# Optimization experiments

Measured on AMD Instinct MI355X. Metric: run time of the kernel, lower is better.

The kernel has to match this reference:

```python
import jax, jax.numpy as jnp
import numpy as np

TOP_K = 5
TEMPERATURE = 0.1
EPS = 1e-12


def _normalize(x):
    # F.normalize(x, dim=-1): x / max(||x||, eps)
    n = jnp.linalg.norm(x, axis=-1, keepdims=True)
    return x / jnp.maximum(n, EPS)


def setup_inputs() -> dict:
    key = jax.random.key(0)
    k1, k2, k3 = jax.random.split(key, 3)
    B, N, D = 1024, 200000, 128
    query = jax.random.normal(k1, (B, D), dtype=jnp.float32)
    # memory bank stores L2-normalized keys (MemoryBank.build applies F.normalize)
    memory = _normalize(jax.random.normal(k2, (N, D), dtype=jnp.float32))
    index_map = jnp.arange(N, dtype=jnp.int64)
    exclude_indices = jax.random.randint(k3, (B,), 0, N, dtype=jnp.int64)
    return {"query": query, "memory": memory, "index_map": index_map,
            "exclude_indices": exclude_indices}


def reference(query, memory, index_map, exclude_indices):
    # cosine similarity: normalize query, memory is already normalized
    qn = _normalize(query)                       # [B, D]
    sim = qn @ memory.T                          # [B, N]
    # exclude own training sample (training-time self-exclusion)
    mask = exclude_indices[:, None] == index_map[None, :]   # [B, N]
    sim = jnp.where(mask, -jnp.inf, sim)
    # top-k (effective_top_k = min(top_k, N-1) = TOP_K here)
    top_sim, top_idx = jax.lax.top_k(sim, TOP_K)             # [B, K]
    weights = jax.nn.softmax(top_sim / TEMPERATURE, axis=-1)  # [B, K]
    vecs = memory[top_idx]                                   # [B, K, D]
    retrieved = jnp.einsum('bk,bkd->bd', weights, vecs)      # weighted sum
    retrieved = _normalize(retrieved)
    distances = 1.0 - top_sim[:, 0]                          # [B]
    return retrieved, distances, weights
```

## Files before the change

### kernel.cpp

```cpp
#include <hip/hip_runtime.h>
#include <hip/hip_bf16.h>
#include <math.h>

#define D128 128
#define TOPK 5
#define NP 200704
#define NCH2 12544
#define NSTRIP 392
#define MARGIN 0.008f
#define CAP 1024
#define SCAP 96
#define SCST 34

typedef __attribute__((ext_vector_type(8))) short short8;
typedef __attribute__((ext_vector_type(4))) float f32x4;

__device__ __forceinline__ short f2bf(float f) {
    union { float f; unsigned u; } c; c.f = f;
    unsigned u = c.u + 0x7FFFu + ((c.u >> 16) & 1u);
    return (short)(u >> 16);
}

__device__ __forceinline__ unsigned pkbf(float x, float y) {
    __hip_bfloat162 h = __float22bfloat162_rn(make_float2(x, y));
    unsigned u; __builtin_memcpy(&u, &h, 4);
    return u;
}
__device__ __forceinline__ unsigned pkh(float a, float b) {
    union { _Float16 h[2]; unsigned u; } c;
    c.h[0] = (_Float16)a; c.h[1] = (_Float16)b; return c.u;
}

template <int NN>
__device__ __forceinline__ void insertg(float (&v)[NN], int (&x)[NN], float nv, int nj) {
    bool g[NN];
    #pragma unroll
    for (int i = 0; i < NN; ++i) g[i] = nv > v[i];
    #pragma unroll
    for (int i = NN - 1; i > 0; --i) {
        v[i] = g[i - 1] ? v[i - 1] : (g[i] ? nv : v[i]);
        x[i] = g[i - 1] ? x[i - 1] : (g[i] ? nj : x[i]);
    }
    v[0] = g[0] ? nv : v[0];
    x[0] = g[0] ? nj : x[0];
}
template <int NN>
__device__ __forceinline__ void insertv(float (&v)[NN], float nv) {
    bool g[NN];
    #pragma unroll
    for (int i = 0; i < NN; ++i) g[i] = nv > v[i];
    #pragma unroll
    for (int i = NN - 1; i > 0; --i)
        v[i] = g[i - 1] ? v[i - 1] : (g[i] ? nv : v[i]);
    v[0] = g[0] ? nv : v[0];
}

__global__ void qnorm_kernel(const float* __restrict__ q, float* __restrict__ qn,
                             short* __restrict__ qbf) {
    int b = blockIdx.x, t = threadIdx.x;
    float v0 = q[(size_t)b * D128 + t];
    float v1 = q[(size_t)b * D128 + t + 64];
    float ss = v0 * v0 + v1 * v1;
    #pragma unroll
    for (int off = 32; off > 0; off >>= 1) ss += __shfl_xor(ss, off, 64);
    float scale = 1.0f / fmaxf(sqrtf(ss), 1e-12f);
    float a0 = v0 * scale, a1 = v1 * scale;
    qn[(size_t)b * D128 + t] = a0;
    qn[(size_t)b * D128 + t + 64] = a1;
    qbf[(size_t)b * D128 + t] = f2bf(a0);
    qbf[(size_t)b * D128 + t + 64] = f2bf(a1);
}

#define MFMA16(a, b, c) __builtin_amdgcn_mfma_f32_16x16x32_bf16(a, b, c, 0, 0, 0)

__global__ __launch_bounds__(256, 3) void simtopk_max(
    const short* __restrict__ qbf, const float* __restrict__ mem,
    _Float16* __restrict__ candT, _Float16* __restrict__ stripT, int N) {
    __shared__ short sK[2][64 * 136];
    __shared__ _Float16 sC[256 * SCST];
    const int b = blockIdx.x;
    const int strip = (b & 7) + ((b >> 5) << 3);
    const int qsg = (b >> 3) & 3;
    const int t = threadIdx.x, w = t >> 6, lane = t & 63;
    const int n = lane & 15, quad = lane >> 4;
    const bool qb0 = (quad & 1) != 0, qb1 = (quad & 2) != 0;
    const int qbase = qsg * 256 + w * 64;

    short8 bq[4][4];
    #pragma unroll
    for (int f = 0; f < 4; ++f) {
        const short* qrow = qbf + (size_t)(qbase + f * 16 + n) * D128 + quad * 8;
        #pragma unroll
        for (int s = 0; s < 4; ++s) bq[f][s] = *(const short8*)(qrow + s * 32);
    }

    const size_t k0 = (size_t)strip * 512;
    const int srow = t >> 4, scol = t & 15;
    const float* gbase = mem + (k0 + srow) * (size_t)D128 + scol * 8;
    const bool tail = (k0 + 512 > (size_t)N);

    float4 fa[8];

    auto loadg = [&](int g) {
        const float* base = gbase + (size_t)g * 64 * D128;
        #pragma unroll
        for (int i = 0; i < 4; ++i) {
            const float4* p = (const float4*)(base + (size_t)i * 16 * D128);
            if (tail) {
                size_t key = k0 + (size_t)(g * 64 + srow + i * 16);
                if (key >= (size_t)N) p = (const float4*)mem;
            }
            fa[2 * i]     = p[0];
            fa[2 * i + 1] = p[1];
        }
    };
    auto storesk = [&](int g, int buf) {
        #pragma unroll
        for (int i = 0; i < 4; ++i) {
            uint4 wv;
            wv.x = pkbf(fa[2 * i].x,     fa[2 * i].y);
            wv.y = pkbf(fa[2 * i].z,     fa[2 * i].w);
            wv.z = pkbf(fa[2 * i + 1].x, fa[2 * i + 1].y);
            wv.w = pkbf(fa[2 * i + 1].z, fa[2 * i + 1].w);
            if (tail && (k0 + (size_t)(g * 64 + srow + i * 16) >= (size_t)N))
                wv = make_uint4(0, 0, 0, 0);
            *((uint4*)&sK[buf][(srow + 16 * i) * 136 + scol * 8]) = wv;
        }
    };

    loadg(0);
    storesk(0, 0);
    __syncthreads();
    loadg(1);

    const int qloc = w * 64 + quad * 16 + n;
    unsigned* sCrow = (unsigned*)((char*)sC + qloc * (SCST * 2));

    for (int round = 0; round < 8; ++round) {
        if (round < 7) storesk(round + 1, (round + 1) & 1);
        if (round < 6) loadg(round + 2);

        const short* kb = sK[round & 1];
        float fin[4];
        #pragma unroll
        for (int tt = 0; tt < 4; ++tt) {
            const short* ab = &kb[(tt * 16 + n) * 136 + quad * 8];
            short8 a0 = *(const short8*)(ab);
            short8 a1 = *(const short8*)(ab + 32);
            short8 a2 = *(const short8*)(ab + 64);
            short8 a3 = *(const short8*)(ab + 96);
            f32x4 c0 = {0.f, 0.f, 0.f, 0.f}, c1 = c0, c2 = c0, c3 = c0;
            c0 = MFMA16(a0, bq[0][0], c0);
            c1 = MFMA16(a0, bq[1][0], c1);
            c2 = MFMA16(a0, bq[2][0], c2);
            c3 = MFMA16(a0, bq[3][0], c3);
            c0 = MFMA16(a1, bq[0][1], c0);
            c1 = MFMA16(a1, bq[1][1], c1);
            c2 = MFMA16(a1, bq[2][1], c2);
            c3 = MFMA16(a1, bq[3][1], c3);
            c0 = MFMA16(a2, bq[0][2], c0);
            c1 = MFMA16(a2, bq[1][2], c1);
            c2 = MFMA16(a2, bq[2][2], c2);
            c3 = MFMA16(a2, bq[3][2], c3);
            c0 = MFMA16(a3, bq[0][3], c0);
            c1 = MFMA16(a3, bq[1][3], c1);
            c2 = MFMA16(a3, bq[2][3], c2);
            c3 = MFMA16(a3, bq[3][3], c3);
            float m0 = fmaxf(fmaxf(c0[0], c0[1]), fmaxf(c0[2], c0[3]));
            float m1 = fmaxf(fmaxf(c1[0], c1[1]), fmaxf(c1[2], c1[3]));
            float m2 = fmaxf(fmaxf(c2[0], c2[1]), fmaxf(c2[2], c2[3]));
            float m3 = fmaxf(fmaxf(c3[0], c3[1]), fmaxf(c3[2], c3[3]));
            float u0 = qb0 ? m1 : m0, u1 = qb0 ? m0 : m1;
            float u2 = qb0 ? m3 : m2, u3 = qb0 ? m2 : m3;
            float v0 = qb1 ? u2 : u0, v1 = qb1 ? u3 : u1;
            float v2 = qb1 ? u0 : u2, v3 = qb1 ? u1 : u3;
            float A = fmaxf(v0, __shfl_xor(v2, 32, 64));
            float B = fmaxf(v1, __shfl_xor(v3, 32, 64));
            fin[tt] = fmaxf(A, __shfl_xor(B, 16, 64));
        }
        sCrow[round * 2]     = pkh(fin[0], fin[1]);
        sCrow[round * 2 + 1] = pkh(fin[2], fin[3]);
        __syncthreads();
    }

    {
        int q = qsg * 256 + t;
        unsigned* gdst = (unsigned*)((short*)candT + (size_t)q * NCH2 + strip * 32);
        const unsigned* row = (const unsigned*)((const char*)sC + t * (SCST * 2));
        float mx = -3e38f;
        #pragma unroll
        for (int j = 0; j < 4; ++j) {
            unsigned u0 = row[4 * j], u1 = row[4 * j + 1];
            unsigned u2 = row[4 * j + 2], u3 = row[4 * j + 3];
            uint4 v; v.x = u0; v.y = u1; v.z = u2; v.w = u3;
            *(uint4*)(gdst + 4 * j) = v;
            unsigned uu[4] = {u0, u1, u2, u3};
            #pragma unroll
            for (int e = 0; e < 4; ++e) {
                unsigned short ha = (unsigned short)(uu[e] & 0xffff);
                unsigned short hb = (unsigned short)(uu[e] >> 16);
                _Float16 f0, f1;
                __builtin_memcpy(&f0, &ha, 2); __builtin_memcpy(&f1, &hb, 2);
                mx = fmaxf(mx, fmaxf((float)f0, (float)f1));
            }
        }
        stripT[(size_t)q * NSTRIP + strip] = (_Float16)mx;
    }
}

__global__ __launch_bounds__(256, 4) void finalize_batch(
    const _Float16* __restrict__ candT, const _Float16* __restrict__ stripT,
    const float* __restrict__ mem, const float* __restrict__ qn,
    const int* __restrict__ index_map, const int* __restrict__ excl,
    float* __restrict__ outR, float* __restrict__ outD, float* __restrict__ outW, int N) {
    const int q = blockIdx.x, t = threadIdx.x;
    const int w = t >> 6, lane = t & 63;

    __shared__ __align__(16) float sQ[D128];
    __shared__ __align__(16) _Float16 sS[NSTRIP];
    __shared__ unsigned short sStr[SCAP];
    __shared__ unsigned short sList[CAP];
    __shared__ int sScnt, sSov, sCnt, sOv;
    __shared__ float sThr;
    __shared__ float sMrg[4 * 6];
    __shared__ float sWv[4 * TOPK];
    __shared__ int   sWk[4 * TOPK];
    __shared__ float sW[TOPK];
    __shared__ int   sJ[TOPK];

    if (t < 128) sQ[t] = qn[(size_t)q * D128 + t];
    if (t == 0) { sScnt = 0; sSov = 0; sCnt = 0; sOv = 0; }
    if (t < NSTRIP / 8)
        *(short8*)(&sS[t * 8]) =
            *(const short8*)((const short*)stripT + (size_t)q * NSTRIP + t * 8);
    __syncthreads();

    float pv[6];
    #pragma unroll
    for (int i = 0; i < 6; ++i) pv[i] = -3e38f;
    for (int i = t; i < NSTRIP; i += 256) {
        float v = (float)sS[i];
        if (v > pv[5]) insertv<6>(pv, v);
    }
    #pragma unroll
    for (int r = 0; r < 6; ++r) {
        float bv = pv[0];
        #pragma unroll
        for (int off = 32; off > 0; off >>= 1) bv = fmaxf(bv, __shfl_xor(bv, off, 64));
        int ml = (pv[0] == bv) ? lane : 64;
        #pragma unroll
        for (int off = 32; off > 0; off >>= 1) ml = min(ml, __shfl_xor(ml, off, 64));
        if (lane == ml) {
            #pragma unroll
            for (int i = 0; i < 5; ++i) pv[i] = pv[i + 1];
            pv[5] = -3e38f;
        }
        if (lane == 0) sMrg[w * 6 + r] = bv;
    }
    __syncthreads();
    if (t == 0) {
        float b6[6];
        #pragma unroll
        for (int i = 0; i < 6; ++i) b6[i] = -3e38f;
        for (int j = 0; j < 24; ++j) {
            float v = sMrg[j];
            if (v > b6[5]) insertv<6>(b6, v);
        }
        sThr = b6[5] - 2.0f * MARGIN;
    }
    __syncthreads();

    const float thr = sThr;
    for (int i = t; i < NSTRIP; i += 256) {
        if ((float)sS[i] >= thr) {
            int p = atomicAdd(&sScnt, 1);
            if (p < SCAP) sStr[p] = (unsigned short)i; else sSov = 1;
        }
    }
    __syncthreads();
    const int scnt = min(sScnt, SCAP);

    if (!sSov) {
        for (int base = 0; base < scnt; base += 8) {
            int si = base + (t >> 5);
            if (si < scnt) {
                int ch = (int)sStr[si] * 32 + (t & 31);
                float v = (float)candT[(size_t)q * NCH2 + ch];
                if (v >= thr) {
                    int p = atomicAdd(&sCnt, 1);
                    if (p < CAP) sList[p] = (unsigned short)ch; else sOv = 1;
                }
            }
        }
    }
    __syncthreads();
    const int ov = (sSov || sOv) ? 1 : 0;
    const int cnt = ov ? NCH2 : min(sCnt, CAP);

    const int exq = excl[q];
    float tv[TOPK]; int ti[TOPK];
    #pragma unroll
    for (int i = 0; i < TOPK; ++i) { tv[i] = -3e38f; ti[i] = -1; }
    const int rounds = (cnt + 15) >> 4;
    for (int r = 0; r < rounds; ++r) {
        int slot = r * 16 + (t >> 4);
        int ch = (slot < cnt) ? (ov ? slot : (int)sList[slot]) : -1;
        int key = ch * 16 + (t & 15);
        float v = -3e38f;
        if (ch >= 0 && key < N && index_map[key] != exq) {
            const float4* mr = (const float4*)(mem + (size_t)key * D128);
            const float4* qv = (const float4*)sQ;
            float acc = 0.f;
            #pragma unroll
            for (int d = 0; d < 32; ++d) {
                float4 a = mr[d], b = qv[d];
                acc += a.x * b.x + a.y * b.y + a.z * b.z + a.w * b.w;
            }
            v = acc;
        }
        if (v > tv[TOPK - 1]) insertg<TOPK>(tv, ti, v, key);
    }

    #pragma unroll
    for (int r = 0; r < TOPK; ++r) {
        float bv = tv[0]; int bk = ti[0];
        #pragma unroll
        for (int off = 32; off > 0; off >>= 1) {
            float ovv = __shfl_xor(bv, off, 64);
            int   okk = __shfl_xor(bk, off, 64);
            if (ovv > bv || (ovv == bv && (unsigned)okk < (unsigned)bk)) { bv = ovv; bk = okk; }
        }
        if (tv[0] == bv && ti[0] == bk) {
            #pragma unroll
            for (int i = 0; i < TOPK - 1; ++i) { tv[i] = tv[i + 1]; ti[i] = ti[i + 1]; }
            tv[TOPK - 1] = -3e38f; ti[TOPK - 1] = -1;
        }
        if (lane == 0) { sWv[w * TOPK + r] = bv; sWk[w * TOPK + r] = bk; }
    }
    __syncthreads();
    if (t == 0) {
        float bv[TOPK]; int bi[TOPK];
        #pragma unroll
        for (int i = 0; i < TOPK; ++i) { bv[i] = -3e38f; bi[i] = -1; }
        for (int j = 0; j < 4 * TOPK; ++j) {
            float v = sWv[j];
            if (v > bv[TOPK - 1]) insertg<TOPK>(bv, bi, v, sWk[j]);
        }
        float m = bv[0], ex[TOPK], sum = 0.f;
        #pragma unroll
        for (int k = 0; k < TOPK; ++k) { ex[k] = __expf((bv[k] - m) * 10.0f); sum += ex[k]; }
        float inv = 1.0f / sum;
        #pragma unroll
        for (int k = 0; k < TOPK; ++k) {
            float wk = ex[k] * inv;
            sW[k] = wk; sJ[k] = bi[k];
            outW[(size_t)q * TOPK + k] = wk;
        }
        outD[q] = 1.0f - bv[0];
    }
    __syncthreads();
    if (t < 64) {
        float r0 = 0.f, r1 = 0.f;
        #pragma unroll
        for (int k = 0; k < TOPK; ++k) {
            const float* mr = mem + (size_t)sJ[k] * D128;
            r0 += sW[k] * mr[t];
            r1 += sW[k] * mr[t + 64];
        }
        float ss = r0 * r0 + r1 * r1;
        #pragma unroll
        for (int off = 32; off > 0; off >>= 1) ss += __shfl_xor(ss, off, 64);
        float scale = 1.0f / fmaxf(sqrtf(ss), 1e-12f);
        outR[(size_t)q * D128 + t]      = r0 * scale;
        outR[(size_t)q * D128 + t + 64] = r1 * scale;
    }
}

extern "C" void kernel_launch(void* const* d_in, const int* in_sizes, int n_in,
                              void* d_out, int out_size, void* d_ws, size_t ws_size,
                              hipStream_t stream) {
    const float* query  = (const float*)d_in[0];
    const float* memory = (const float*)d_in[1];
    const int* index_map = (const int*)d_in[2];
    const int* excl      = (const int*)d_in[3];

    const int B = in_sizes[3];
    const int N = in_sizes[2];

    char* ws = (char*)d_ws;
    float*    qn     = (float*)(ws);
    short*    qbf    = (short*)(ws + 524288);
    _Float16* candT  = (_Float16*)(ws + 786432);
    _Float16* stripT = (_Float16*)(ws + 786432 + 25690112);

    float* outR = (float*)d_out;
    float* outD = outR + (size_t)B * D128;
    float* outW = outD + B;

    qnorm_kernel<<<B, 64, 0, stream>>>(query, qn, qbf);
    simtopk_max<<<NSTRIP * 4, 256, 0, stream>>>(qbf, memory, candT, stripT, N);
    finalize_batch<<<B, 256, 0, stream>>>(candT, stripT, memory, qn, index_map, excl,
                                          outR, outD, outW, N);
}
```

Before: 247.1 us.

## Switch similarity MFMA to 32x32x16 tiles with single-buffered LDS staging

Replaces the 16x16x32 bf16 MFMA tiling with 32x32x16 MFMAs, so each wave computes two 32-query by 32-key blocks per key tile and reduces each to per-16-key chunk maxima with fewer cross-lane shuffles. The bf16 conversion now happens right after the global load, so the prefetch registers hold packed bf16 instead of fp32, and the double-buffered LDS key tile becomes a single buffer. This lowers register and LDS pressure and the per-tile reduction overhead, but adds an extra barrier per round and removes the overlap between LDS stores and MFMA work.

After: 255.0 us. 1.03x slower.

```diff
diff --git a/kernel.cpp b/kernel.cpp
--- a/kernel.cpp
+++ b/kernel.cpp
@@ -14,6 +14,7 @@
 
 typedef __attribute__((ext_vector_type(8))) short short8;
 typedef __attribute__((ext_vector_type(4))) float f32x4;
+typedef __attribute__((ext_vector_type(16))) float f32x16;
 
 __device__ __forceinline__ short f2bf(float f) {
     union { float f; unsigned u; } c; c.f = f;
@@ -71,27 +72,26 @@
     qbf[(size_t)b * D128 + t + 64] = f2bf(a1);
 }
 
-#define MFMA16(a, b, c) __builtin_amdgcn_mfma_f32_16x16x32_bf16(a, b, c, 0, 0, 0)
+#define MFMA32(a, b, c) __builtin_amdgcn_mfma_f32_32x32x16_bf16(a, b, c, 0, 0, 0)
 
 __global__ __launch_bounds__(256, 3) void simtopk_max(
     const short* __restrict__ qbf, const float* __restrict__ mem,
     _Float16* __restrict__ candT, _Float16* __restrict__ stripT, int N) {
-    __shared__ short sK[2][64 * 136];
+    __shared__ short sK[64 * 136];
     __shared__ _Float16 sC[256 * SCST];
     const int b = blockIdx.x;
     const int strip = (b & 7) + ((b >> 5) << 3);
     const int qsg = (b >> 3) & 3;
     const int t = threadIdx.x, w = t >> 6, lane = t & 63;
-    const int n = lane & 15, quad = lane >> 4;
-    const bool qb0 = (quad & 1) != 0, qb1 = (quad & 2) != 0;
+    const int l31 = lane & 31, lh = lane >> 5;
     const int qbase = qsg * 256 + w * 64;
 
-    short8 bq[4][4];
-    #pragma unroll
-    for (int f = 0; f < 4; ++f) {
-        const short* qrow = qbf + (size_t)(qbase + f * 16 + n) * D128 + quad * 8;
-        #pragma unroll
-        for (int s = 0; s < 4; ++s) bq[f][s] = *(const short8*)(qrow + s * 32);
+    short8 bq[2][8];
+    #pragma unroll
+    for (int f = 0; f < 2; ++f) {
+        const short* qrow = qbf + (size_t)(qbase + f * 32 + l31) * D128 + lh * 8;
+        #pragma unroll
+        for (int s = 0; s < 8; ++s) bq[f][s] = *(const short8*)(qrow + s * 16);
     }
 
     const size_t k0 = (size_t)strip * 512;
@@ -99,90 +99,75 @@
     const float* gbase = mem + (k0 + srow) * (size_t)D128 + scol * 8;
     const bool tail = (k0 + 512 > (size_t)N);
 
-    float4 fa[8];
-
-    auto loadg = [&](int g) {
+    uint4 fb[4];
+
+    auto loadcv = [&](int g) {
         const float* base = gbase + (size_t)g * 64 * D128;
         #pragma unroll
         for (int i = 0; i < 4; ++i) {
             const float4* p = (const float4*)(base + (size_t)i * 16 * D128);
+            bool oob = false;
             if (tail) {
                 size_t key = k0 + (size_t)(g * 64 + srow + i * 16);
-                if (key >= (size_t)N) p = (const float4*)mem;
-            }
-            fa[2 * i]     = p[0];
-            fa[2 * i + 1] = p[1];
+                if (key >= (size_t)N) { p = (const float4*)mem; oob = true; }
+            }
+            float4 x = p[0], y = p[1];
+            uint4 wv;
+            wv.x = pkbf(x.x, x.y); wv.y = pkbf(x.z, x.w);
+            wv.z = pkbf(y.x, y.y); wv.w = pkbf(y.z, y.w);
+            if (oob) wv = make_uint4(0, 0, 0, 0);
+            fb[i] = wv;
         }
     };
-    auto storesk = [&](int g, int buf) {
-        #pragma unroll
-        for (int i = 0; i < 4; ++i) {
-            uint4 wv;
-            wv.x = pkbf(fa[2 * i].x,     fa[2 * i].y);
-            wv.y = pkbf(fa[2 * i].z,     fa[2 * i].w);
-            wv.z = pkbf(fa[2 * i + 1].x, fa[2 * i + 1].y);
-            wv.w = pkbf(fa[2 * i + 1].z, fa[2 * i + 1].w);
-            if (tail && (k0 + (size_t)(g * 64 + srow + i * 16) >= (size_t)N))
-                wv = make_uint4(0, 0, 0, 0);
-            *((uint4*)&sK[buf][(srow + 16 * i) * 136 + scol * 8]) = wv;
-        }
+    auto storesk = [&]() {
+        #pragma unroll
+        for (int i = 0; i < 4; ++i)
+            *((uint4*)&sK[(srow + 16 * i) * 136 + scol * 8]) = fb[i];
     };
 
-    loadg(0);
-    storesk(0, 0);
-    __syncthreads();
-    loadg(1);
-
-    const int qloc = w * 64 + quad * 16 + n;
-    unsigned* sCrow = (unsigned*)((char*)sC + qloc * (SCST * 2));
+    loadcv(0);
+    storesk();
+    __syncthreads();
+    loadcv(1);
+
+    auto reduce_write = [&](const f32x16& ac, int f, int kt, int round) {
+        float pA = fmaxf(fmaxf(fmaxf(ac[0], ac[1]), fmaxf(ac[2], ac[3])),
+                         fmaxf(fmaxf(ac[4], ac[5]), fmaxf(ac[6], ac[7])));
+        float pB = fmaxf(fmaxf(fmaxf(ac[8], ac[9]), fmaxf(ac[10], ac[11])),
+                         fmaxf(fmaxf(ac[12], ac[13]), fmaxf(ac[14], ac[15])));
+        pA = fmaxf(pA, __shfl_xor(pA, 32, 64));
+        pB = fmaxf(pB, __shfl_xor(pB, 32, 64));
+        if (lane < 32) {
+            int qloc = w * 64 + f * 32 + l31;
+            unsigned* p = (unsigned*)((char*)sC + qloc * (SCST * 2));
+            p[round * 2 + kt] = pkh(pA, pB);
+        }
+    };
 
     for (int round = 0; round < 8; ++round) {
-        if (round < 7) storesk(round + 1, (round + 1) & 1);
-        if (round < 6) loadg(round + 2);
-
-        const short* kb = sK[round & 1];
-        float fin[4];
-        #pragma unroll
-        for (int tt = 0; tt < 4; ++tt) {
-            const short* ab = &kb[(tt * 16 + n) * 136 + quad * 8];
-            short8 a0 = *(const short8*)(ab);
-            short8 a1 = *(const short8*)(ab + 32);
-            short8 a2 = *(const short8*)(ab + 64);
-            short8 a3 = *(const short8*)(ab + 96);
-            f32x4 c0 = {0.f, 0.f, 0.f, 0.f}, c1 = c0, c2 = c0, c3 = c0;
-            c0 = MFMA16(a0, bq[0][0], c0);
-            c1 = MFMA16(a0, bq[1][0], c1);
-            c2 = MFMA16(a0, bq[2][0], c2);
-            c3 = MFMA16(a0, bq[3][0], c3);
-            c0 = MFMA16(a1, bq[0][1], c0);
-            c1 = MFMA16(a1, bq[1][1], c1);
-            c2 = MFMA16(a1, bq[2][1], c2);
-            c3 = MFMA16(a1, bq[3][1], c3);
-            c0 = MFMA16(a2, bq[0][2], c0);
-            c1 = MFMA16(a2, bq[1][2], c1);
-            c2 = MFMA16(a2, bq[2][2], c2);
-            c3 = MFMA16(a2, bq[3][2], c3);
-            c0 = MFMA16(a3, bq[0][3], c0);
-            c1 = MFMA16(a3, bq[1][3], c1);
-            c2 = MFMA16(a3, bq[2][3], c2);
-            c3 = MFMA16(a3, bq[3][3], c3);
-            float m0 = fmaxf(fmaxf(c0[0], c0[1]), fmaxf(c0[2], c0[3]));
-            float m1 = fmaxf(fmaxf(c1[0], c1[1]), fmaxf(c1[2], c1[3]));
-            float m2 = fmaxf(fmaxf(c2[0], c2[1]), fmaxf(c2[2], c2[3]));
-            float m3 = fmaxf(fmaxf(c3[0], c3[1]), fmaxf(c3[2], c3[3]));
-            float u0 = qb0 ? m1 : m0, u1 = qb0 ? m0 : m1;
-            float u2 = qb0 ? m3 : m2, u3 = qb0 ? m2 : m3;
-            float v0 = qb1 ? u2 : u0, v1 = qb1 ? u3 : u1;
-            float v2 = qb1 ? u0 : u2, v3 = qb1 ? u1 : u3;
-            float A = fmaxf(v0, __shfl_xor(v2, 32, 64));
-            float B = fmaxf(v1, __shfl_xor(v3, 32, 64));
-            fin[tt] = fmaxf(A, __shfl_xor(B, 16, 64));
-        }
-        sCrow[round * 2]     = pkh(fin[0], fin[1]);
-        sCrow[round * 2 + 1] = pkh(fin[2], fin[3]);
-        __syncthreads();
-    }
-
+        #pragma unroll
+        for (int kt = 0; kt < 2; ++kt) {
+            const short* arow = &sK[(kt * 32 + l31) * 136 + lh * 8];
+            f32x16 acc0 = {0.f,0.f,0.f,0.f,0.f,0.f,0.f,0.f,0.f,0.f,0.f,0.f,0.f,0.f,0.f,0.f};
+            f32x16 acc1 = acc0;
+            #pragma unroll
+            for (int s = 0; s < 8; ++s) {
+                short8 a = *(const short8*)(arow + s * 16);
+                acc0 = MFMA32(a, bq[0][s], acc0);
+                acc1 = MFMA32(a, bq[1][s], acc1);
+            }
+            reduce_write(acc0, 0, kt, round);
+            reduce_write(acc1, 1, kt, round);
+        }
+        if (round < 7) {
+            __syncthreads();
+            storesk();
+            __syncthreads();
+            if (round < 6) loadcv(round + 2);
+        }
+    }
+
+    __syncthreads();
     {
         int q = qsg * 256 + t;
         unsigned* gdst = (unsigned*)((short*)candT + (size_t)q * NCH2 + strip * 32);
```

## Convert keys to bf16 at load time and drop LDS candidate staging

Applied to the files above, without the earlier changes.

Converts each prefetched fp32 memory row to packed bf16 right after the global load. This roughly halves the registers held for the in-flight prefetch. It also removes the shared-memory staging buffer for per-chunk maxima: each round now writes its candidate maxima straight to global memory, and the strip maximum is kept in a register. The aim is to cut LDS footprint and register pressure and to drop the final copy-out pass. The cost is that the bf16 conversion must wait for the loads inside the same round, which can expose global latency. The candidate writes also become narrower, strided 8-byte stores.

Measured after the change: 280.6 us. +13.5%, slower.

```diff
diff --git a/kernel.cpp b/kernel.cpp
--- a/kernel.cpp
+++ b/kernel.cpp
@@ -10,7 +10,6 @@
 #define MARGIN 0.008f
 #define CAP 1024
 #define SCAP 96
-#define SCST 34
 
 typedef __attribute__((ext_vector_type(8))) short short8;
 typedef __attribute__((ext_vector_type(4))) float f32x4;
@@ -77,7 +76,6 @@
     const short* __restrict__ qbf, const float* __restrict__ mem,
     _Float16* __restrict__ candT, _Float16* __restrict__ stripT, int N) {
     __shared__ short sK[2][64 * 136];
-    __shared__ _Float16 sC[256 * SCST];
     const int b = blockIdx.x;
     const int strip = (b & 7) + ((b >> 5) << 3);
     const int qsg = (b >> 3) & 3;
@@ -85,6 +83,7 @@
     const int n = lane & 15, quad = lane >> 4;
     const bool qb0 = (quad & 1) != 0, qb1 = (quad & 2) != 0;
     const int qbase = qsg * 256 + w * 64;
+    const int myq = qbase + quad * 16 + n;
 
     short8 bq[4][4];
     #pragma unroll
@@ -99,46 +98,43 @@
     const float* gbase = mem + (k0 + srow) * (size_t)D128 + scol * 8;
     const bool tail = (k0 + 512 > (size_t)N);
 
-    float4 fa[8];
-
-    auto loadg = [&](int g) {
+    uint4 fb[4];
+
+    auto loadcv = [&](int g) {
         const float* base = gbase + (size_t)g * 64 * D128;
         #pragma unroll
         for (int i = 0; i < 4; ++i) {
             const float4* p = (const float4*)(base + (size_t)i * 16 * D128);
+            bool oob = false;
             if (tail) {
                 size_t key = k0 + (size_t)(g * 64 + srow + i * 16);
-                if (key >= (size_t)N) p = (const float4*)mem;
+                if (key >= (size_t)N) { p = (const float4*)mem; oob = true; }
             }
-            fa[2 * i]     = p[0];
-            fa[2 * i + 1] = p[1];
+            float4 x = p[0], y = p[1];
+            uint4 wv;
+            wv.x = pkbf(x.x, x.y); wv.y = pkbf(x.z, x.w);
+            wv.z = pkbf(y.x, y.y); wv.w = pkbf(y.z, y.w);
+            if (oob) wv = make_uint4(0, 0, 0, 0);
+            fb[i] = wv;
         }
     };
-    auto storesk = [&](int g, int buf) {
-        #pragma unroll
-        for (int i = 0; i < 4; ++i) {
-            uint4 wv;
-            wv.x = pkbf(fa[2 * i].x,     fa[2 * i].y);
-            wv.y = pkbf(fa[2 * i].z,     fa[2 * i].w);
-            wv.z = pkbf(fa[2 * i + 1].x, fa[2 * i + 1].y);
-            wv.w = pkbf(fa[2 * i + 1].z, fa[2 * i + 1].w);
-            if (tail && (k0 + (size_t)(g * 64 + srow + i * 16) >= (size_t)N))
-                wv = make_uint4(0, 0, 0, 0);
-            *((uint4*)&sK[buf][(srow + 16 * i) * 136 + scol * 8]) = wv;
-        }
+    auto storesk = [&](int buf) {
+        #pragma unroll
+        for (int i = 0; i < 4; ++i)
+            *((uint4*)&sK[buf][(srow + 16 * i) * 136 + scol * 8]) = fb[i];
     };
 
-    loadg(0);
-    storesk(0, 0);
-    __syncthreads();
-    loadg(1);
-
-    const int qloc = w * 64 + quad * 16 + n;
-    unsigned* sCrow = (unsigned*)((char*)sC + qloc * (SCST * 2));
+    loadcv(0);
+    storesk(0);
+    __syncthreads();
+    loadcv(1);
+
+    float mx = -3e38f;
+    short* crow = (short*)candT + (size_t)myq * NCH2 + strip * 32;
 
     for (int round = 0; round < 8; ++round) {
-        if (round < 7) storesk(round + 1, (round + 1) & 1);
-        if (round < 6) loadg(round + 2);
+        if (round < 7) storesk((round + 1) & 1);
+        if (round < 6) loadcv(round + 2);
 
         const short* kb = sK[round & 1];
         float fin[4];
@@ -178,34 +174,12 @@
             float B = fmaxf(v1, __shfl_xor(v3, 32, 64));
             fin[tt] = fmaxf(A, __shfl_xor(B, 16, 64));
         }
-        sCrow[round * 2]     = pkh(fin[0], fin[1]);
-        sCrow[round * 2 + 1] = pkh(fin[2], fin[3]);
+        uint2 pk; pk.x = pkh(fin[0], fin[1]); pk.y = pkh(fin[2], fin[3]);
+        *(uint2*)(crow + round * 4) = pk;
+        mx = fmaxf(mx, fmaxf(fmaxf(fin[0], fin[1]), fmaxf(fin[2], fin[3])));
         __syncthreads();
     }
-
-    {
-        int q = qsg * 256 + t;
-        unsigned* gdst = (unsigned*)((short*)candT + (size_t)q * NCH2 + strip * 32);
-        const unsigned* row = (const unsigned*)((const char*)sC + t * (SCST * 2));
-        float mx = -3e38f;
-        #pragma unroll
-        for (int j = 0; j < 4; ++j) {
-            unsigned u0 = row[4 * j], u1 = row[4 * j + 1];
-            unsigned u2 = row[4 * j + 2], u3 = row[4 * j + 3];
-            uint4 v; v.x = u0; v.y = u1; v.z = u2; v.w = u3;
-            *(uint4*)(gdst + 4 * j) = v;
-            unsigned uu[4] = {u0, u1, u2, u3};
-            #pragma unroll
-            for (int e = 0; e < 4; ++e) {
-                unsigned short ha = (unsigned short)(uu[e] & 0xffff);
-                unsigned short hb = (unsigned short)(uu[e] >> 16);
-                _Float16 f0, f1;
-                __builtin_memcpy(&f0, &ha, 2); __builtin_memcpy(&f1, &hb, 2);
-                mx = fmaxf(mx, fmaxf((float)f0, (float)f1));
-            }
-        }
-        stripT[(size_t)q * NSTRIP + strip] = (_Float16)mx;
-    }
+    stripT[(size_t)myq * NSTRIP + strip] = (_Float16)mx;
 }
 
 __global__ __launch_bounds__(256, 4) void finalize_batch(
```

## Halve strip size per block, doubling grid and using single-buffered LDS

Applied to the files above, without the earlier changes.

Each similarity block now covers 256 memory keys instead of 512, so the grid doubles to 3136 blocks and the strip-max summary gets twice as many entries per query. The double-buffered key tile in shared memory becomes a single buffer with an extra barrier per round. The finalize kernel is adjusted to scan 784 strip maxima with a larger strip-candidate cap and 16-chunk strips. The intent is better occupancy and load balance from smaller LDS use and more blocks. The cost is that each block reloads the query fragments for half as many keys, there is less load/compute overlap, and there is more strip-selection work.

Result: no change. 250.6 us (+1.4%).

```diff
diff --git a/kernel.cpp b/kernel.cpp
--- a/kernel.cpp
+++ b/kernel.cpp
@@ -7,10 +7,11 @@
 #define NP 200704
 #define NCH2 12544
 #define NSTRIP 392
+#define NSTRIP2 784
 #define MARGIN 0.008f
 #define CAP 1024
-#define SCAP 96
-#define SCST 34
+#define SCAP 192
+#define SCC 18
 
 typedef __attribute__((ext_vector_type(8))) short short8;
 typedef __attribute__((ext_vector_type(4))) float f32x4;
@@ -76,11 +77,13 @@
 __global__ __launch_bounds__(256, 3) void simtopk_max(
     const short* __restrict__ qbf, const float* __restrict__ mem,
     _Float16* __restrict__ candT, _Float16* __restrict__ stripT, int N) {
-    __shared__ short sK[2][64 * 136];
-    __shared__ _Float16 sC[256 * SCST];
+    __shared__ short sK[64 * 136];
+    __shared__ _Float16 sC[256 * SCC];
     const int b = blockIdx.x;
-    const int strip = (b & 7) + ((b >> 5) << 3);
-    const int qsg = (b >> 3) & 3;
+    const int strip = (b & 7) + ((b >> 6) << 3);
+    const int sub = (b >> 3) & 7;
+    const int qsg = sub >> 1;
+    const int h = sub & 1;
     const int t = threadIdx.x, w = t >> 6, lane = t & 63;
     const int n = lane & 15, quad = lane >> 4;
     const bool qb0 = (quad & 1) != 0, qb1 = (quad & 2) != 0;
@@ -94,10 +97,10 @@
         for (int s = 0; s < 4; ++s) bq[f][s] = *(const short8*)(qrow + s * 32);
     }
 
-    const size_t k0 = (size_t)strip * 512;
+    const size_t k0 = (size_t)strip * 512 + (size_t)h * 256;
     const int srow = t >> 4, scol = t & 15;
     const float* gbase = mem + (k0 + srow) * (size_t)D128 + scol * 8;
-    const bool tail = (k0 + 512 > (size_t)N);
+    const bool tail = (k0 + 256 > (size_t)N);
 
     float4 fa[8];
 
@@ -114,7 +117,7 @@
             fa[2 * i + 1] = p[1];
         }
     };
-    auto storesk = [&](int g, int buf) {
+    auto storesk = [&](int g) {
         #pragma unroll
         for (int i = 0; i < 4; ++i) {
             uint4 wv;
@@ -124,27 +127,23 @@
             wv.w = pkbf(fa[2 * i + 1].z, fa[2 * i + 1].w);
             if (tail && (k0 + (size_t)(g * 64 + srow + i * 16) >= (size_t)N))
                 wv = make_uint4(0, 0, 0, 0);
-            *((uint4*)&sK[buf][(srow + 16 * i) * 136 + scol * 8]) = wv;
+            *((uint4*)&sK[(srow + 16 * i) * 136 + scol * 8]) = wv;
         }
     };
 
     loadg(0);
-    storesk(0, 0);
+    storesk(0);
     __syncthreads();
     loadg(1);
 
     const int qloc = w * 64 + quad * 16 + n;
-    unsigned* sCrow = (unsigned*)((char*)sC + qloc * (SCST * 2));
-
-    for (int round = 0; round < 8; ++round) {
-        if (round < 7) storesk(round + 1, (round + 1) & 1);
-        if (round < 6) loadg(round + 2);
-
-        const short* kb = sK[round & 1];
+    unsigned* sCrow = (unsigned*)((char*)sC + qloc * (SCC * 2));
+
+    for (int round = 0; round < 4; ++round) {
         float fin[4];
         #pragma unroll
         for (int tt = 0; tt < 4; ++tt) {
-            const short* ab = &kb[(tt * 16 + n) * 136 + quad * 8];
+            const short* ab = &sK[(tt * 16 + n) * 136 + quad * 8];
             short8 a0 = *(const short8*)(ab);
             short8 a1 = *(const short8*)(ab + 32);
             short8 a2 = *(const short8*)(ab + 64);
@@ -180,31 +179,36 @@
         }
         sCrow[round * 2]     = pkh(fin[0], fin[1]);
         sCrow[round * 2 + 1] = pkh(fin[2], fin[3]);
-        __syncthreads();
-    }
-
+        if (round < 3) {
+            __syncthreads();
+            storesk(round + 1);
+            __syncthreads();
+            if (round < 2) loadg(round + 2);
+        }
+    }
+
+    __syncthreads();
     {
         int q = qsg * 256 + t;
-        unsigned* gdst = (unsigned*)((short*)candT + (size_t)q * NCH2 + strip * 32);
-        const unsigned* row = (const unsigned*)((const char*)sC + t * (SCST * 2));
+        unsigned* gdst = (unsigned*)((short*)candT + (size_t)q * NCH2
+                                     + strip * 32 + h * 16);
+        const unsigned* row = (const unsigned*)((const char*)sC + t * (SCC * 2));
         float mx = -3e38f;
-        #pragma unroll
-        for (int j = 0; j < 4; ++j) {
-            unsigned u0 = row[4 * j], u1 = row[4 * j + 1];
-            unsigned u2 = row[4 * j + 2], u3 = row[4 * j + 3];
-            uint4 v; v.x = u0; v.y = u1; v.z = u2; v.w = u3;
-            *(uint4*)(gdst + 4 * j) = v;
-            unsigned uu[4] = {u0, u1, u2, u3};
-            #pragma unroll
-            for (int e = 0; e < 4; ++e) {
-                unsigned short ha = (unsigned short)(uu[e] & 0xffff);
-                unsigned short hb = (unsigned short)(uu[e] >> 16);
-                _Float16 f0, f1;
-                __builtin_memcpy(&f0, &ha, 2); __builtin_memcpy(&f1, &hb, 2);
-                mx = fmaxf(mx, fmaxf((float)f0, (float)f1));
-            }
-        }
-        stripT[(size_t)q * NSTRIP + strip] = (_Float16)mx;
+        uint4 v0, v1;
+        v0.x = row[0]; v0.y = row[1]; v0.z = row[2]; v0.w = row[3];
+        v1.x = row[4]; v1.y = row[5]; v1.z = row[6]; v1.w = row[7];
+        *(uint4*)(gdst)     = v0;
+        *(uint4*)(gdst + 4) = v1;
+        unsigned uu[8] = {v0.x, v0.y, v0.z, v0.w, v1.x, v1.y, v1.z, v1.w};
+        #pragma unroll
+        for (int e = 0; e < 8; ++e) {
+            unsigned short ha = (unsigned short)(uu[e] & 0xffff);
+            unsigned short hb = (unsigned short)(uu[e] >> 16);
+            _Float16 f0, f1;
+            __builtin_memcpy(&f0, &ha, 2); __builtin_memcpy(&f1, &hb, 2);
+            mx = fmaxf(mx, fmaxf((float)f0, (float)f1));
+        }
+        stripT[(size_t)q * NSTRIP2 + strip * 2 + h] = (_Float16)mx;
     }
 }
 
@@ -217,7 +221,7 @@
     const int w = t >> 6, lane = t & 63;
 
     __shared__ __align__(16) float sQ[D128];
-    __shared__ __align__(16) _Float16 sS[NSTRIP];
+    __shared__ __align__(16) _Float16 sS[NSTRIP2];
     __shared__ unsigned short sStr[SCAP];
     __shared__ unsigned short sList[CAP];
     __shared__ int sScnt, sSov, sCnt, sOv;
@@ -230,15 +234,15 @@
 
     if (t < 128) sQ[t] = qn[(size_t)q * D128 + t];
     if (t == 0) { sScnt = 0; sSov = 0; sCnt = 0; sOv = 0; }
-    if (t < NSTRIP / 8)
+    if (t < NSTRIP2 / 8)
         *(short8*)(&sS[t * 8]) =
-            *(const short8*)((const short*)stripT + (size_t)q * NSTRIP + t * 8);
+            *(const short8*)((const short*)stripT + (size_t)q * NSTRIP2 + t * 8);
     __syncthreads();
 
     float pv[6];
     #pragma unroll
     for (int i = 0; i < 6; ++i) pv[i] = -3e38f;
-    for (int i = t; i < NSTRIP; i += 256) {
+    for (int i = t; i < NSTRIP2; i += 256) {
         float v = (float)sS[i];
         if (v > pv[5]) insertv<6>(pv, v);
     }
@@ -271,7 +275,7 @@
     __syncthreads();
 
     const float thr = sThr;
-    for (int i = t; i < NSTRIP; i += 256) {
+    for (int i = t; i < NSTRIP2; i += 256) {
         if ((float)sS[i] >= thr) {
             int p = atomicAdd(&sScnt, 1);
             if (p < SCAP) sStr[p] = (unsigned short)i; else sSov = 1;
@@ -281,10 +285,10 @@
     const int scnt = min(sScnt, SCAP);
 
     if (!sSov) {
-        for (int base = 0; base < scnt; base += 8) {
-            int si = base + (t >> 5);
+        for (int base = 0; base < scnt; base += 16) {
+            int si = base + (t >> 4);
             if (si < scnt) {
-                int ch = (int)sStr[si] * 32 + (t & 31);
+                int ch = (int)sStr[si] * 16 + (t & 15);
                 float v = (float)candT[(size_t)q * NCH2 + ch];
                 if (v >= thr) {
                     int p = atomicAdd(&sCnt, 1);
@@ -398,7 +402,7 @@
     float* outW = outD + B;
 
     qnorm_kernel<<<B, 64, 0, stream>>>(query, qn, qbf);
-    simtopk_max<<<NSTRIP * 4, 256, 0, stream>>>(qbf, memory, candT, stripT, N);
+    simtopk_max<<<NSTRIP * 8, 256, 0, stream>>>(qbf, memory, candT, stripT, N);
     finalize_batch<<<B, 256, 0, stream>>>(candT, stripT, memory, qn, index_map, excl,
                                           outR, outD, outW, N);
 }
```
